# Kernel tuning notes

Hardware: AMD Instinct MI355X
Metric: run time of the kernel (lower is better)

Reference implementation:

```python
import jax, jax.numpy as jnp
import numpy as np

NUM_HEADS = 4
HEAD_DIM = 32
QUERY_DIM = 256
KEY_DIM = 128
INNER = NUM_HEADS * HEAD_DIM  # 128


def setup_inputs() -> dict:
    key = jax.random.key(0)
    ks = jax.random.split(key, 8)
    B, T, D, H, W = 2, 4, QUERY_DIM, 40, 40
    C, Hm, Wm = KEY_DIM, 40, 40
    query = jax.random.normal(ks[0], (B, T, D, H, W), dtype=jnp.float32)
    k_in = jax.random.normal(ks[1], (B, T, C, Hm, Wm), dtype=jnp.float32)
    v_in = jax.random.normal(ks[2], (B, T, C, Hm, Wm), dtype=jnp.float32)
    # Linear weights stored as (in, out); torch nn.Linear init ~ U(-1/sqrt(in), 1/sqrt(in))
    def lin(k, fan_in, fan_out):
        bound = 1.0 / np.sqrt(fan_in)
        return jax.random.uniform(k, (fan_in, fan_out), minval=-bound, maxval=bound, dtype=jnp.float32)
    Wq = lin(ks[3], QUERY_DIM, INNER)
    Wk = lin(ks[4], KEY_DIM, INNER)
    Wv = lin(ks[5], KEY_DIM, INNER)
    Wo = lin(ks[6], INNER, QUERY_DIM)
    bo = jax.random.uniform(ks[7], (QUERY_DIM,), minval=-1.0 / np.sqrt(INNER), maxval=1.0 / np.sqrt(INNER), dtype=jnp.float32)
    return {"query": query, "key": k_in, "value": v_in,
            "Wq": Wq, "Wk": Wk, "Wv": Wv, "Wo": Wo, "bo": bo}


def reference(query, key, value, Wq, Wk, Wv, Wo, bo):
    B, T, D, H, W = query.shape
    _, _, C, Hm, Wm = key.shape
    scale = HEAD_DIM ** (-0.5)
    # b t d h w -> b t (h w) d
    q = query.reshape(B, T, D, H * W).transpose(0, 1, 3, 2)
    k = key.reshape(B, T, C, Hm * Wm).transpose(0, 1, 3, 2)
    v = value.reshape(B, T, C, Hm * Wm).transpose(0, 1, 3, 2)
    # projections then split heads: b t n (h d) -> b t h n d
    def heads(x):
        Bn, Tn, N, _ = x.shape
        return x.reshape(Bn, Tn, N, NUM_HEADS, HEAD_DIM).transpose(0, 1, 3, 2, 4)
    Q = heads(q @ Wq)
    K = heads(k @ Wk)
    V = heads(v @ Wv)
    scores = jnp.einsum('bthqd,bthkd->bthqk', Q, K) * scale
    probs = jax.nn.softmax(scores, axis=-1)
    out = jnp.einsum('bthqk,bthkd->bthqd', probs, V)
    # b t h n d -> b t n (h d)
    out = out.transpose(0, 1, 3, 2, 4).reshape(B, T, H * W, INNER)
    fused = out @ Wo + bo
    # b t (h w) d -> b t d h w
    return fused.transpose(0, 1, 3, 2).reshape(B, T, D, H, W)
```

## Files before the change

### kernel.cpp

```cpp
#include <hip/hip_runtime.h>

#define NTOK 1600
#define BT_TOTAL 8
#define INNER 128
#define HD 32
#define NH 4
#define QDIM 256

typedef short short8 __attribute__((ext_vector_type(8)));
typedef short short4v __attribute__((ext_vector_type(4)));
typedef float f32x4 __attribute__((ext_vector_type(4)));
typedef float f32x16 __attribute__((ext_vector_type(16)));

__device__ inline short f2b(float x) {
  union { float f; unsigned u; } v; v.f = x;
  unsigned r = (v.u + 0x7FFF + ((v.u >> 16) & 1)) >> 16;
  return (short)r;
}
__device__ inline unsigned bpack2(float a, float b) {
  union { float f; unsigned u; } ua, ub;
  ua.f = a; ub.f = b;
  return __builtin_amdgcn_perm(ub.u + 0x8000u, ua.u + 0x8000u, 0x07060302u);
}
__device__ inline short8 ldsfrag(const short* p) {
  short4v a = *(const short4v*)p;
  short4v b = *(const short4v*)(p + 4);
  short8 r;
  r[0] = a[0]; r[1] = a[1]; r[2] = a[2]; r[3] = a[3];
  r[4] = b[0]; r[5] = b[1]; r[6] = b[2]; r[7] = b[3];
  return r;
}
__device__ inline short8 mk8(unsigned a, unsigned b, unsigned c, unsigned d) {
  union { unsigned u[4]; short8 v; } t;
  t.u[0] = a; t.u[1] = b; t.u[2] = c; t.u[3] = d;
  return t.v;
}

__global__ __launch_bounds__(256) void proj_fused(
    const float* __restrict__ query, const float* __restrict__ Wq,
    const float* __restrict__ key, const float* __restrict__ Wk,
    const float* __restrict__ value, const float* __restrict__ Wv,
    short* __restrict__ Qbf, short* __restrict__ Kbf,
    short* __restrict__ Vbf) {
  const int n0 = blockIdx.x * 64;
  const int which = blockIdx.y;
  const int bt = blockIdx.z;
  const int t = threadIdx.x;
  const int lane = t & 63, w = t >> 6;
  const int quad = lane >> 4, n16 = lane & 15;

  const float* X; const float* Wt; short* Y; int nchunk; float scl;
  if (which == 0) {
    X = query; Wt = Wq; Y = Qbf; nchunk = 8; scl = 0.17677669529663687f;
  } else if (which == 1) {
    X = key; Wt = Wk; Y = Kbf; nchunk = 4; scl = 1.0f;
  } else {
    X = value; Wt = Wv; Y = Vbf; nchunk = 4; scl = 1.0f;
  }
  const float* Xb = X + (size_t)bt * (nchunk * 32) * NTOK;

  __shared__ short Xs[64 * 36];
  __shared__ short Ws[128 * 36];

  f32x4 acc[8];
#pragma unroll
  for (int i = 0; i < 8; ++i) acc[i] = (f32x4){0.f, 0.f, 0.f, 0.f};

  const int iw = t & 127, g = t >> 7;

  float xf0[4], xf1[4], wf0[8], wf1[8];
  auto loadX = [&](int cd) {
#pragma unroll
    for (int dp = 0; dp < 4; ++dp) {
      int dl = w * 8 + dp * 2;
      xf0[dp] = Xb[(size_t)(cd + dl) * NTOK + n0 + lane];
      xf1[dp] = Xb[(size_t)(cd + dl + 1) * NTOK + n0 + lane];
    }
  };
  auto loadW = [&](int cd) {
#pragma unroll
    for (int dp = 0; dp < 8; ++dp) {
      int dl = g * 16 + dp * 2;
      wf0[dp] = Wt[(size_t)(cd + dl) * INNER + iw];
      wf1[dp] = Wt[(size_t)(cd + dl + 1) * INNER + iw];
    }
  };
  loadX(0); loadW(0);

  for (int c = 0; c < nchunk; ++c) {
#pragma unroll
    for (int dp = 0; dp < 4; ++dp)
      *(unsigned*)&Xs[lane * 36 + w * 8 + dp * 2] = bpack2(xf0[dp], xf1[dp]);
#pragma unroll
    for (int dp = 0; dp < 8; ++dp)
      *(unsigned*)&Ws[iw * 36 + g * 16 + dp * 2] = bpack2(wf0[dp], wf1[dp]);
    __syncthreads();
    if (c + 1 < nchunk) { loadX((c + 1) * 32); loadW((c + 1) * 32); }
    if (which != 2) {
      short8 a[4], b[2];
#pragma unroll
      for (int tg = 0; tg < 4; ++tg)
        a[tg] = ldsfrag(&Xs[(tg * 16 + n16) * 36 + quad * 8]);
#pragma unroll
      for (int cg = 0; cg < 2; ++cg)
        b[cg] = ldsfrag(&Ws[(w * 32 + cg * 16 + n16) * 36 + quad * 8]);
#pragma unroll
      for (int tg = 0; tg < 4; ++tg)
#pragma unroll
        for (int cg = 0; cg < 2; ++cg)
          acc[tg * 2 + cg] = __builtin_amdgcn_mfma_f32_16x16x32_bf16(
              a[tg], b[cg], acc[tg * 2 + cg], 0, 0, 0);
    } else {
      short8 a[2], b[4];
#pragma unroll
      for (int ig = 0; ig < 2; ++ig)
        a[ig] = ldsfrag(&Ws[(w * 32 + ig * 16 + n16) * 36 + quad * 8]);
#pragma unroll
      for (int tg = 0; tg < 4; ++tg)
        b[tg] = ldsfrag(&Xs[(tg * 16 + n16) * 36 + quad * 8]);
#pragma unroll
      for (int ig = 0; ig < 2; ++ig)
#pragma unroll
        for (int tg = 0; tg < 4; ++tg)
          acc[ig * 4 + tg] = __builtin_amdgcn_mfma_f32_16x16x32_bf16(
              a[ig], b[tg], acc[ig * 4 + tg], 0, 0, 0);
    }
    __syncthreads();
  }

  if (which != 2) {
    short* Yb = Y + ((size_t)bt * NH + w) * NTOK * HD;
#pragma unroll
    for (int tg = 0; tg < 4; ++tg)
#pragma unroll
      for (int cg = 0; cg < 2; ++cg) {
        f32x4 a = acc[tg * 2 + cg];
#pragma unroll
        for (int r = 0; r < 4; ++r) {
          int tok = n0 + tg * 16 + quad * 4 + r;
          Yb[(size_t)tok * HD + cg * 16 + n16] = f2b(a[r] * scl);
        }
      }
  } else {
#pragma unroll
    for (int ig = 0; ig < 2; ++ig)
#pragma unroll
      for (int tg = 0; tg < 4; ++tg) {
        f32x4 a = acc[ig * 4 + tg];
#pragma unroll
        for (int r = 0; r < 4; ++r) {
          int irow = w * 32 + ig * 16 + quad * 4 + r;
          Y[((size_t)bt * INNER + irow) * NTOK + n0 + tg * 16 + n16] =
              f2b(a[r]);
        }
      }
  }
}

__global__ __launch_bounds__(256, 5) void attn_mfma(
    const short* __restrict__ Qb, const short* __restrict__ Kb,
    const short* __restrict__ Vb, short* __restrict__ Obf) {
  const int id = blockIdx.x;
  const int qt = id >> 5;
  const int pair = id & 31;
  const int bt = pair >> 2, h = pair & 3;
  const int wave = threadIdx.x >> 6, lane = threadIdx.x & 63;
  const int lh = lane >> 5, q32 = lane & 31;
  const int q0 = qt * 32;
  const size_t btok = ((size_t)bt * NH + h) * NTOK;
  const size_t bd = ((size_t)bt * NH + h) * HD;
  const bool hi = (lane >= 32);

  __shared__ float Cb[2][17][64];

  const short* Qp = &Qb[(btok + q0 + q32) * HD + lh * 8];
  const short8 bq0 = *(const short8*)(Qp);
  const short8 bq1 = *(const short8*)(Qp + 16);

  const int kstart = wave * 416 - (wave == 3 ? 32 : 0);
  const int nch = 13 - (wave >> 1);
  const short* Kp = &Kb[(btok + kstart + q32) * HD + lh * 8];
  const short* Vp = &Vb[(bd + q32) * NTOK + kstart + lh * 8];

  f32x16 o = {0.f, 0.f, 0.f, 0.f, 0.f, 0.f, 0.f, 0.f,
              0.f, 0.f, 0.f, 0.f, 0.f, 0.f, 0.f, 0.f};
  float lsum = 0.f;

  short8 ak0 = *(const short8*)(Kp);
  short8 ak1 = *(const short8*)(Kp + 16);

  for (int i = 0; i < nch; ++i) {
    const int kc = i * 32;
    const int kn = (i + 1 < nch) ? kc + 32 : 0;
    short8 nk0 = *(const short8*)(Kp + (size_t)kn * HD);
    short8 nk1 = *(const short8*)(Kp + (size_t)kn * HD + 16);
    short8 av0 = *(const short8*)(Vp + kc);
    short8 av1 = *(const short8*)(Vp + kc + 16);

    f32x16 s = __builtin_amdgcn_mfma_f32_32x32x16_bf16(
        ak0, bq0,
        (f32x16){0.f, 0.f, 0.f, 0.f, 0.f, 0.f, 0.f, 0.f,
                 0.f, 0.f, 0.f, 0.f, 0.f, 0.f, 0.f, 0.f},
        0, 0, 0);
    s = __builtin_amdgcn_mfma_f32_32x32x16_bf16(ak1, bq1, s, 0, 0, 0);

    unsigned Pd[8];
#pragma unroll
    for (int g = 0; g < 4; ++g) {
      float e0 = __expf(s[4 * g + 0]);
      float e1 = __expf(s[4 * g + 1]);
      float e2 = __expf(s[4 * g + 2]);
      float e3 = __expf(s[4 * g + 3]);
      lsum += (e0 + e1) + (e2 + e3);
      Pd[2 * g + 0] = bpack2(e0, e1);
      Pd[2 * g + 1] = bpack2(e2, e3);
    }
    unsigned Xd[8];
#pragma unroll
    for (int j = 0; j < 8; ++j)
      Xd[j] = (unsigned)__shfl_xor((int)Pd[j], 32);
    short8 pb0 = mk8(hi ? Xd[2] : Pd[0], hi ? Xd[3] : Pd[1],
                     hi ? Pd[2] : Xd[0], hi ? Pd[3] : Xd[1]);
    short8 pb1 = mk8(hi ? Xd[6] : Pd[4], hi ? Xd[7] : Pd[5],
                     hi ? Pd[6] : Xd[4], hi ? Pd[7] : Xd[5]);

    o = __builtin_amdgcn_mfma_f32_32x32x16_bf16(av0, pb0, o, 0, 0, 0);
    o = __builtin_amdgcn_mfma_f32_32x32x16_bf16(av1, pb1, o, 0, 0, 0);
    ak0 = nk0; ak1 = nk1;
  }

  lsum += __shfl_xor(lsum, 32);

  auto dump = [&](int sidx) {
#pragma unroll
    for (int r = 0; r < 16; ++r) Cb[sidx][r][lane] = o[r];
    Cb[sidx][16][lane] = lsum;
  };
  auto accum = [&](int sidx) {
#pragma unroll
    for (int r = 0; r < 16; ++r) o[r] += Cb[sidx][r][lane];
    lsum += Cb[sidx][16][lane];
  };
  if (wave == 1) dump(0);
  if (wave == 3) dump(1);
  __syncthreads();
  if (wave == 0) accum(0);
  if (wave == 2) accum(1);
  __syncthreads();
  if (wave == 2) dump(0);
  __syncthreads();
  if (wave == 0) {
    accum(0);
    const float inv = 1.f / lsum;
    short* Op = &Obf[((size_t)bt * NTOK + q0 + q32) * INNER + h * HD + lh * 4];
#pragma unroll
    for (int g = 0; g < 4; ++g) {
      unsigned d0 = bpack2(o[4 * g + 0] * inv, o[4 * g + 1] * inv);
      unsigned d1 = bpack2(o[4 * g + 2] * inv, o[4 * g + 3] * inv);
      *(uint2*)&Op[8 * g] = make_uint2(d0, d1);
    }
  }
}

__global__ __launch_bounds__(256) void oproj_mfma(
    const short* __restrict__ Obf, const float* __restrict__ Wo,
    const float* __restrict__ bo, float* __restrict__ out) {
  const int tok0 = blockIdx.x * 64, d0 = blockIdx.y * 64;
  const int bt = blockIdx.z;
  const int t = threadIdx.x, lane = t & 63, w = t >> 6;
  const int quad = lane >> 4, n16 = lane & 15;
  __shared__ short Wos[64 * 36];
  f32x4 acc[4];
#pragma unroll
  for (int i = 0; i < 4; ++i) acc[i] = (f32x4){0.f, 0.f, 0.f, 0.f};
  const int tok = tok0 + w * 16 + n16;

  float wf0[4], wf1[4];
  short8 bfr;
  auto loadWo = [&](int c) {
#pragma unroll
    for (int dp = 0; dp < 4; ++dp) {
      int il = w * 8 + dp * 2;
      wf0[dp] = Wo[(size_t)(c * 32 + il) * QDIM + d0 + lane];
      wf1[dp] = Wo[(size_t)(c * 32 + il + 1) * QDIM + d0 + lane];
    }
  };
  auto loadB = [&](int c) {
    bfr = *(const short8*)&Obf[((size_t)bt * NTOK + tok) * INNER + c * 32 +
                               quad * 8];
  };
  loadWo(0); loadB(0);

  for (int c = 0; c < 4; ++c) {
#pragma unroll
    for (int dp = 0; dp < 4; ++dp)
      *(unsigned*)&Wos[lane * 36 + w * 8 + dp * 2] = bpack2(wf0[dp], wf1[dp]);
    __syncthreads();
    short8 b0 = bfr;
    if (c < 3) { loadWo(c + 1); loadB(c + 1); }
#pragma unroll
    for (int ag = 0; ag < 4; ++ag) {
      short8 a = ldsfrag(&Wos[(ag * 16 + n16) * 36 + quad * 8]);
      acc[ag] = __builtin_amdgcn_mfma_f32_16x16x32_bf16(a, b0, acc[ag], 0, 0, 0);
    }
    __syncthreads();
  }

#pragma unroll
  for (int ag = 0; ag < 4; ++ag) {
    f32x4 a = acc[ag];
#pragma unroll
    for (int r = 0; r < 4; ++r) {
      int dout = d0 + ag * 16 + quad * 4 + r;
      out[((size_t)bt * QDIM + dout) * NTOK + tok] = a[r] + bo[dout];
    }
  }
}

extern "C" void kernel_launch(void* const* d_in, const int* in_sizes, int n_in,
                              void* d_out, int out_size, void* d_ws,
                              size_t ws_size, hipStream_t stream) {
  const float* query = (const float*)d_in[0];
  const float* key = (const float*)d_in[1];
  const float* value = (const float*)d_in[2];
  const float* Wq = (const float*)d_in[3];
  const float* Wk = (const float*)d_in[4];
  const float* Wv = (const float*)d_in[5];
  const float* Wo = (const float*)d_in[6];
  const float* bo = (const float*)d_in[7];
  float* out = (float*)d_out;

  const size_t arr = (size_t)BT_TOTAL * INNER * NTOK;
  short* Qbf = (short*)d_ws;
  short* Kbf = Qbf + arr;
  short* Vbf = Kbf + arr;
  short* Obf = Vbf + arr;

  proj_fused<<<dim3(25, 3, BT_TOTAL), 256, 0, stream>>>(
      query, Wq, key, Wk, value, Wv, Qbf, Kbf, Vbf);
  attn_mfma<<<dim3(1600), 256, 0, stream>>>(Qbf, Kbf, Vbf, Obf);
  oproj_mfma<<<dim3(25, 4, BT_TOTAL), 256, 0, stream>>>(Obf, Wo, bo, out);
}
```

Before: 132.7 us.

## Replace LDS-tiled projection GEMMs with per-wave direct-load 32x32 MFMA kernels

The Q/K/V projection and output projection kernels stop staging tiles in shared memory and no longer use block-wide barriers. Each wave now computes its own 32x32 output tile, loading fp32 operands straight from global memory, packing them to bf16 in registers, and issuing 32x32x16 MFMAs. This removes LDS traffic and synchronisation and gives finer-grained work distribution. In exchange, data is no longer reused across waves within a block, so global and L2 load traffic rises, and the strided fp32 loads of weights and activations may coalesce poorly.

New measurement: 165.4 us. 1.25x slower.

```diff
diff --git a/kernel.cpp b/kernel.cpp
--- a/kernel.cpp
+++ b/kernel.cpp
@@ -22,138 +22,83 @@
   ua.f = a; ub.f = b;
   return __builtin_amdgcn_perm(ub.u + 0x8000u, ua.u + 0x8000u, 0x07060302u);
 }
-__device__ inline short8 ldsfrag(const short* p) {
-  short4v a = *(const short4v*)p;
-  short4v b = *(const short4v*)(p + 4);
-  short8 r;
-  r[0] = a[0]; r[1] = a[1]; r[2] = a[2]; r[3] = a[3];
-  r[4] = b[0]; r[5] = b[1]; r[6] = b[2]; r[7] = b[3];
-  return r;
-}
 __device__ inline short8 mk8(unsigned a, unsigned b, unsigned c, unsigned d) {
   union { unsigned u[4]; short8 v; } t;
   t.u[0] = a; t.u[1] = b; t.u[2] = c; t.u[3] = d;
   return t.v;
 }
-
-__global__ __launch_bounds__(256) void proj_fused(
+__device__ inline f32x16 zero16() {
+  return (f32x16){0.f, 0.f, 0.f, 0.f, 0.f, 0.f, 0.f, 0.f,
+                  0.f, 0.f, 0.f, 0.f, 0.f, 0.f, 0.f, 0.f};
+}
+__device__ inline short8 fragf32(const float* __restrict__ base, int rs,
+                                 int col, int kbase, int lh) {
+  unsigned d[4];
+#pragma unroll
+  for (int e = 0; e < 4; ++e) {
+    float f0 = base[(size_t)(kbase + lh * 8 + 2 * e) * rs + col];
+    float f1 = base[(size_t)(kbase + lh * 8 + 2 * e + 1) * rs + col];
+    d[e] = bpack2(f0, f1);
+  }
+  return mk8(d[0], d[1], d[2], d[3]);
+}
+
+__global__ __launch_bounds__(256) void proj_direct(
     const float* __restrict__ query, const float* __restrict__ Wq,
     const float* __restrict__ key, const float* __restrict__ Wk,
     const float* __restrict__ value, const float* __restrict__ Wv,
     short* __restrict__ Qbf, short* __restrict__ Kbf,
     short* __restrict__ Vbf) {
-  const int n0 = blockIdx.x * 64;
-  const int which = blockIdx.y;
-  const int bt = blockIdx.z;
-  const int t = threadIdx.x;
-  const int lane = t & 63, w = t >> 6;
-  const int quad = lane >> 4, n16 = lane & 15;
-
-  const float* X; const float* Wt; short* Y; int nchunk; float scl;
+  const int wave = threadIdx.x >> 6, lane = threadIdx.x & 63;
+  const int lh = lane >> 5, q32 = lane & 31;
+  const int wg = blockIdx.x * 4 + wave;
+  const int which = wg / 1600;
+  int rem = wg - which * 1600;
+  const int bt = rem / 200;
+  const int t8 = rem - bt * 200;
+  const int ot = t8 / 50;
+  const int tt = t8 - ot * 50;
+
+  const float* aBase; const float* bBase;
+  int aStride, bStride, aCol, bCol, nk;
   if (which == 0) {
-    X = query; Wt = Wq; Y = Qbf; nchunk = 8; scl = 0.17677669529663687f;
+    aBase = query + (size_t)bt * QDIM * NTOK; aStride = NTOK;
+    aCol = tt * 32 + q32;
+    bBase = Wq; bStride = INNER; bCol = ot * 32 + q32; nk = 16;
   } else if (which == 1) {
-    X = key; Wt = Wk; Y = Kbf; nchunk = 4; scl = 1.0f;
+    aBase = key + (size_t)bt * INNER * NTOK; aStride = NTOK;
+    aCol = tt * 32 + q32;
+    bBase = Wk; bStride = INNER; bCol = ot * 32 + q32; nk = 8;
   } else {
-    X = value; Wt = Wv; Y = Vbf; nchunk = 4; scl = 1.0f;
-  }
-  const float* Xb = X + (size_t)bt * (nchunk * 32) * NTOK;
-
-  __shared__ short Xs[64 * 36];
-  __shared__ short Ws[128 * 36];
-
-  f32x4 acc[8];
-#pragma unroll
-  for (int i = 0; i < 8; ++i) acc[i] = (f32x4){0.f, 0.f, 0.f, 0.f};
-
-  const int iw = t & 127, g = t >> 7;
-
-  float xf0[4], xf1[4], wf0[8], wf1[8];
-  auto loadX = [&](int cd) {
-#pragma unroll
-    for (int dp = 0; dp < 4; ++dp) {
-      int dl = w * 8 + dp * 2;
-      xf0[dp] = Xb[(size_t)(cd + dl) * NTOK + n0 + lane];
-      xf1[dp] = Xb[(size_t)(cd + dl + 1) * NTOK + n0 + lane];
-    }
-  };
-  auto loadW = [&](int cd) {
-#pragma unroll
-    for (int dp = 0; dp < 8; ++dp) {
-      int dl = g * 16 + dp * 2;
-      wf0[dp] = Wt[(size_t)(cd + dl) * INNER + iw];
-      wf1[dp] = Wt[(size_t)(cd + dl + 1) * INNER + iw];
-    }
-  };
-  loadX(0); loadW(0);
-
-  for (int c = 0; c < nchunk; ++c) {
-#pragma unroll
-    for (int dp = 0; dp < 4; ++dp)
-      *(unsigned*)&Xs[lane * 36 + w * 8 + dp * 2] = bpack2(xf0[dp], xf1[dp]);
-#pragma unroll
-    for (int dp = 0; dp < 8; ++dp)
-      *(unsigned*)&Ws[iw * 36 + g * 16 + dp * 2] = bpack2(wf0[dp], wf1[dp]);
-    __syncthreads();
-    if (c + 1 < nchunk) { loadX((c + 1) * 32); loadW((c + 1) * 32); }
-    if (which != 2) {
-      short8 a[4], b[2];
-#pragma unroll
-      for (int tg = 0; tg < 4; ++tg)
-        a[tg] = ldsfrag(&Xs[(tg * 16 + n16) * 36 + quad * 8]);
-#pragma unroll
-      for (int cg = 0; cg < 2; ++cg)
-        b[cg] = ldsfrag(&Ws[(w * 32 + cg * 16 + n16) * 36 + quad * 8]);
-#pragma unroll
-      for (int tg = 0; tg < 4; ++tg)
-#pragma unroll
-        for (int cg = 0; cg < 2; ++cg)
-          acc[tg * 2 + cg] = __builtin_amdgcn_mfma_f32_16x16x32_bf16(
-              a[tg], b[cg], acc[tg * 2 + cg], 0, 0, 0);
-    } else {
-      short8 a[2], b[4];
-#pragma unroll
-      for (int ig = 0; ig < 2; ++ig)
-        a[ig] = ldsfrag(&Ws[(w * 32 + ig * 16 + n16) * 36 + quad * 8]);
-#pragma unroll
-      for (int tg = 0; tg < 4; ++tg)
-        b[tg] = ldsfrag(&Xs[(tg * 16 + n16) * 36 + quad * 8]);
-#pragma unroll
-      for (int ig = 0; ig < 2; ++ig)
-#pragma unroll
-        for (int tg = 0; tg < 4; ++tg)
-          acc[ig * 4 + tg] = __builtin_amdgcn_mfma_f32_16x16x32_bf16(
-              a[ig], b[tg], acc[ig * 4 + tg], 0, 0, 0);
-    }
-    __syncthreads();
+    aBase = Wv; aStride = INNER; aCol = ot * 32 + q32;
+    bBase = value + (size_t)bt * INNER * NTOK; bStride = NTOK;
+    bCol = tt * 32 + q32; nk = 8;
+  }
+
+  f32x16 acc = zero16();
+#pragma unroll 4
+  for (int ks = 0; ks < nk; ++ks) {
+    short8 a = fragf32(aBase, aStride, aCol, ks * 16, lh);
+    short8 b = fragf32(bBase, bStride, bCol, ks * 16, lh);
+    acc = __builtin_amdgcn_mfma_f32_32x32x16_bf16(a, b, acc, 0, 0, 0);
   }
 
   if (which != 2) {
-    short* Yb = Y + ((size_t)bt * NH + w) * NTOK * HD;
-#pragma unroll
-    for (int tg = 0; tg < 4; ++tg)
-#pragma unroll
-      for (int cg = 0; cg < 2; ++cg) {
-        f32x4 a = acc[tg * 2 + cg];
-#pragma unroll
-        for (int r = 0; r < 4; ++r) {
-          int tok = n0 + tg * 16 + quad * 4 + r;
-          Yb[(size_t)tok * HD + cg * 16 + n16] = f2b(a[r] * scl);
-        }
-      }
+    short* Yb = ((which == 0) ? Qbf : Kbf) +
+                ((size_t)(bt * NH + ot) * NTOK) * HD;
+    const float scl = (which == 0) ? 0.17677669529663687f : 1.0f;
+    const int tokbase = tt * 32;
+#pragma unroll
+    for (int r = 0; r < 16; ++r) {
+      int row = (r & 3) + 8 * (r >> 2) + 4 * lh;
+      Yb[(size_t)(tokbase + row) * HD + q32] = f2b(acc[r] * scl);
+    }
   } else {
 #pragma unroll
-    for (int ig = 0; ig < 2; ++ig)
-#pragma unroll
-      for (int tg = 0; tg < 4; ++tg) {
-        f32x4 a = acc[ig * 4 + tg];
-#pragma unroll
-        for (int r = 0; r < 4; ++r) {
-          int irow = w * 32 + ig * 16 + quad * 4 + r;
-          Y[((size_t)bt * INNER + irow) * NTOK + n0 + tg * 16 + n16] =
-              f2b(a[r]);
-        }
-      }
+    for (int r = 0; r < 16; ++r) {
+      int irow = ot * 32 + (r & 3) + 8 * (r >> 2) + 4 * lh;
+      Vbf[((size_t)bt * INNER + irow) * NTOK + tt * 32 + q32] = f2b(acc[r]);
+    }
   }
 }
 
@@ -182,8 +127,7 @@
   const short* Kp = &Kb[(btok + kstart + q32) * HD + lh * 8];
   const short* Vp = &Vb[(bd + q32) * NTOK + kstart + lh * 8];
 
-  f32x16 o = {0.f, 0.f, 0.f, 0.f, 0.f, 0.f, 0.f, 0.f,
-              0.f, 0.f, 0.f, 0.f, 0.f, 0.f, 0.f, 0.f};
+  f32x16 o = zero16();
   float lsum = 0.f;
 
   short8 ak0 = *(const short8*)(Kp);
@@ -197,11 +141,8 @@
     short8 av0 = *(const short8*)(Vp + kc);
     short8 av1 = *(const short8*)(Vp + kc + 16);
 
-    f32x16 s = __builtin_amdgcn_mfma_f32_32x32x16_bf16(
-        ak0, bq0,
-        (f32x16){0.f, 0.f, 0.f, 0.f, 0.f, 0.f, 0.f, 0.f,
-                 0.f, 0.f, 0.f, 0.f, 0.f, 0.f, 0.f, 0.f},
-        0, 0, 0);
+    f32x16 s = __builtin_amdgcn_mfma_f32_32x32x16_bf16(ak0, bq0, zero16(),
+                                                       0, 0, 0);
     s = __builtin_amdgcn_mfma_f32_32x32x16_bf16(ak1, bq1, s, 0, 0, 0);
 
     unsigned Pd[8];
@@ -262,58 +203,31 @@
   }
 }
 
-__global__ __launch_bounds__(256) void oproj_mfma(
+__global__ __launch_bounds__(256) void oproj_direct(
     const short* __restrict__ Obf, const float* __restrict__ Wo,
     const float* __restrict__ bo, float* __restrict__ out) {
-  const int tok0 = blockIdx.x * 64, d0 = blockIdx.y * 64;
-  const int bt = blockIdx.z;
-  const int t = threadIdx.x, lane = t & 63, w = t >> 6;
-  const int quad = lane >> 4, n16 = lane & 15;
-  __shared__ short Wos[64 * 36];
-  f32x4 acc[4];
-#pragma unroll
-  for (int i = 0; i < 4; ++i) acc[i] = (f32x4){0.f, 0.f, 0.f, 0.f};
-  const int tok = tok0 + w * 16 + n16;
-
-  float wf0[4], wf1[4];
-  short8 bfr;
-  auto loadWo = [&](int c) {
-#pragma unroll
-    for (int dp = 0; dp < 4; ++dp) {
-      int il = w * 8 + dp * 2;
-      wf0[dp] = Wo[(size_t)(c * 32 + il) * QDIM + d0 + lane];
-      wf1[dp] = Wo[(size_t)(c * 32 + il + 1) * QDIM + d0 + lane];
-    }
-  };
-  auto loadB = [&](int c) {
-    bfr = *(const short8*)&Obf[((size_t)bt * NTOK + tok) * INNER + c * 32 +
-                               quad * 8];
-  };
-  loadWo(0); loadB(0);
-
-  for (int c = 0; c < 4; ++c) {
-#pragma unroll
-    for (int dp = 0; dp < 4; ++dp)
-      *(unsigned*)&Wos[lane * 36 + w * 8 + dp * 2] = bpack2(wf0[dp], wf1[dp]);
-    __syncthreads();
-    short8 b0 = bfr;
-    if (c < 3) { loadWo(c + 1); loadB(c + 1); }
-#pragma unroll
-    for (int ag = 0; ag < 4; ++ag) {
-      short8 a = ldsfrag(&Wos[(ag * 16 + n16) * 36 + quad * 8]);
-      acc[ag] = __builtin_amdgcn_mfma_f32_16x16x32_bf16(a, b0, acc[ag], 0, 0, 0);
-    }
-    __syncthreads();
-  }
-
-#pragma unroll
-  for (int ag = 0; ag < 4; ++ag) {
-    f32x4 a = acc[ag];
-#pragma unroll
-    for (int r = 0; r < 4; ++r) {
-      int dout = d0 + ag * 16 + quad * 4 + r;
-      out[((size_t)bt * QDIM + dout) * NTOK + tok] = a[r] + bo[dout];
-    }
+  const int wave = threadIdx.x >> 6, lane = threadIdx.x & 63;
+  const int lh = lane >> 5, q32 = lane & 31;
+  const int wg = blockIdx.x * 4 + wave;
+  const int bt = wg / 400;
+  int rem = wg - bt * 400;
+  const int dt = rem / 50;
+  const int tt = rem - dt * 50;
+  const int d0 = dt * 32;
+  const int tok = tt * 32 + q32;
+
+  f32x16 acc = zero16();
+#pragma unroll
+  for (int ks = 0; ks < 8; ++ks) {
+    short8 a = fragf32(Wo, QDIM, d0 + q32, ks * 16, lh);
+    short8 b = *(const short8*)&Obf[((size_t)bt * NTOK + tok) * INNER +
+                                    ks * 16 + lh * 8];
+    acc = __builtin_amdgcn_mfma_f32_32x32x16_bf16(a, b, acc, 0, 0, 0);
+  }
+#pragma unroll
+  for (int r = 0; r < 16; ++r) {
+    int row = d0 + (r & 3) + 8 * (r >> 2) + 4 * lh;
+    out[((size_t)bt * QDIM + row) * NTOK + tok] = acc[r] + bo[row];
   }
 }
 
@@ -336,8 +250,8 @@
   short* Vbf = Kbf + arr;
   short* Obf = Vbf + arr;
 
-  proj_fused<<<dim3(25, 3, BT_TOTAL), 256, 0, stream>>>(
-      query, Wq, key, Wk, value, Wv, Qbf, Kbf, Vbf);
+  proj_direct<<<dim3(1200), 256, 0, stream>>>(query, Wq, key, Wk, value, Wv,
+                                              Qbf, Kbf, Vbf);
   attn_mfma<<<dim3(1600), 256, 0, stream>>>(Qbf, Kbf, Vbf, Obf);
-  oproj_mfma<<<dim3(25, 4, BT_TOTAL), 256, 0, stream>>>(Obf, Wo, bo, out);
-}
+  oproj_direct<<<dim3(800), 256, 0, stream>>>(Obf, Wo, bo, out);
+}
```
